# Performance work log

Measured on AMD Instinct MI355X. Metric: run time of the kernel, lower is better.

Reference implementation:

```python
import jax, jax.numpy as jnp
import numpy as np

D_MODEL = 768
N_HEADS = 12
D_HEAD = D_MODEL // N_HEADS
TEMP = float(np.sqrt(D_HEAD))


def setup_inputs() -> dict:
    key = jax.random.key(0)
    ks = jax.random.split(key, 12)
    B, S, D = 8, 2048, D_MODEL
    patches = jax.random.normal(ks[0], (B, S, D), dtype=jnp.float32)
    in_weight = jax.random.uniform(ks[1], (D * 3, D), dtype=jnp.float32)
    in_bias = jax.random.uniform(ks[2], (D * 3,), dtype=jnp.float32)
    out_w = jax.random.normal(ks[3], (D, D), dtype=jnp.float32) * (1.0 / np.sqrt(D))
    out_b = jnp.zeros((D,), dtype=jnp.float32)
    mlp_w1 = jax.random.normal(ks[4], (4 * D, D), dtype=jnp.float32) * (1.0 / np.sqrt(D))
    mlp_b1 = jnp.zeros((4 * D,), dtype=jnp.float32)
    mlp_w2 = jax.random.normal(ks[5], (D, 4 * D), dtype=jnp.float32) * (1.0 / np.sqrt(4 * D))
    mlp_b2 = jnp.zeros((D,), dtype=jnp.float32)
    ln1_g = jnp.ones((D,), dtype=jnp.float32)
    ln1_b = jnp.zeros((D,), dtype=jnp.float32)
    ln2_g = jnp.ones((D,), dtype=jnp.float32)
    ln2_b = jnp.zeros((D,), dtype=jnp.float32)
    return {
        "patches": patches,
        "in_weight": in_weight, "in_bias": in_bias,
        "out_w": out_w, "out_b": out_b,
        "mlp_w1": mlp_w1, "mlp_b1": mlp_b1,
        "mlp_w2": mlp_w2, "mlp_b2": mlp_b2,
        "ln1_g": ln1_g, "ln1_b": ln1_b,
        "ln2_g": ln2_g, "ln2_b": ln2_b,
    }


def layer_norm(x, g, b, eps=1e-5):
    mu = jnp.mean(x, axis=-1, keepdims=True)
    var = jnp.var(x, axis=-1, keepdims=True)
    return (x - mu) * jax.lax.rsqrt(var + eps) * g + b


def mha(x, in_weight, in_bias, out_w, out_b):
    # Replicate quirky per-head reshape: [3D, D] -> [H, d_head, 3, D]
    W = in_weight.reshape(N_HEADS, D_HEAD, 3, D_MODEL)  # h, e, 3, d
    Bv = in_bias.reshape(N_HEADS, D_HEAD, 3)            # h, e, 3
    qw, kw, vw = W[:, :, 0, :], W[:, :, 1, :], W[:, :, 2, :]  # [H, e, D]
    qb, kb, vb = Bv[:, :, 0], Bv[:, :, 1], Bv[:, :, 2]        # [H, e]
    # Q,K,V per head: [B, H, S, e]
    Q = jnp.einsum('bsd,hed->bhse', x, qw) + qb[None, :, None, :]
    K = jnp.einsum('bsd,hed->bhse', x, kw) + kb[None, :, None, :]
    V = jnp.einsum('bsd,hed->bhse', x, vw) + vb[None, :, None, :]
    atn = jnp.einsum('bhse,bhte->bhst', Q, K)
    atn = jax.nn.softmax(atn / TEMP, axis=-1)
    # NOTE: original uses V (not atn @ V) as head output; heads concatenated over feature dim
    B_, H, S, e = V.shape
    heads = jnp.transpose(V, (0, 2, 1, 3)).reshape(B_, S, H * e)
    masks = jnp.sum(atn, axis=1)  # sum over heads: [B, S, S]
    out = heads @ out_w.T + out_b
    return out, masks


def reference(patches, in_weight, in_bias, out_w, out_b,
              mlp_w1, mlp_b1, mlp_w2, mlp_b2,
              ln1_g, ln1_b, ln2_g, ln2_b):
    x = layer_norm(patches, ln1_g, ln1_b)
    sa, _ = mha(x, in_weight, in_bias, out_w, out_b)
    x = sa + x  # dropout = identity (eval)
    x = layer_norm(x, ln2_g, ln2_b)
    h = jax.nn.selu(x @ mlp_w1.T + mlp_b1)
    x = (h @ mlp_w2.T + mlp_b2) + x
    return x
```

## Files before the change

kernel.cpp:

```cpp
#include <hip/hip_runtime.h>


typedef __bf16 bf16;
typedef __bf16 bf16x8 __attribute__((ext_vector_type(8)));
typedef __bf16 bf16x4 __attribute__((ext_vector_type(4)));
typedef float  f32x4  __attribute__((ext_vector_type(4)));

#define N_ROWS  16384

#define AS1(p) ((const __attribute__((address_space(1))) void*)(p))
#define AS3(p) ((__attribute__((address_space(3))) void*)(p))

__global__ __launch_bounds__(256) void cast_kernel(const float* __restrict__ x,
                                                   bf16* __restrict__ y, int n4) {
  int i = blockIdx.x * 256 + threadIdx.x;
  if (i >= n4) return;
  float4 v = ((const float4*)x)[i];
  bf16x4 o = {(bf16)v.x, (bf16)v.y, (bf16)v.z, (bf16)v.w};
  *(bf16x4*)(y + 4 * (size_t)i) = o;
}

__global__ __launch_bounds__(256) void wvt_kernel(const float* __restrict__ in_weight,
                                                  bf16* __restrict__ wvt) {
  int k = blockIdx.x * 256 + threadIdx.x;
  int j = blockIdx.y;
  wvt[(size_t)k * 768 + j] = (bf16)in_weight[((size_t)j * 3 + 2) * 768 + k];
}

__global__ __launch_bounds__(64) void bias_combine_kernel(const float* __restrict__ out_w,
                                                          const float* __restrict__ in_bias,
                                                          const float* __restrict__ out_b,
                                                          float* __restrict__ bc) {
  int n = blockIdx.x, l = threadIdx.x;
  float s = 0.f;
  for (int j = l; j < 768; j += 64) s += out_w[(size_t)n * 768 + j] * in_bias[j * 3 + 2];
#pragma unroll
  for (int off = 32; off > 0; off >>= 1) s += __shfl_xor(s, off, 64);
  if (l == 0) bc[n] = s + out_b[n];
}

__global__ __launch_bounds__(256) void ln_kernel(const float* __restrict__ x,
                                                 const float* __restrict__ g,
                                                 const float* __restrict__ b,
                                                 bf16* __restrict__ y) {
  const int row = blockIdx.x;
  const float* xr = x + (size_t)row * 768;
  float v[3], s1 = 0.f, s2 = 0.f;
#pragma unroll
  for (int i = 0; i < 3; ++i) {
    v[i] = xr[threadIdx.x + i * 256];
    s1 += v[i];
    s2 += v[i] * v[i];
  }
#pragma unroll
  for (int off = 32; off > 0; off >>= 1) {
    s1 += __shfl_xor(s1, off, 64);
    s2 += __shfl_xor(s2, off, 64);
  }
  __shared__ float red[8];
  int w = threadIdx.x >> 6, l = threadIdx.x & 63;
  if (l == 0) { red[w * 2] = s1; red[w * 2 + 1] = s2; }
  __syncthreads();
  s1 = red[0] + red[2] + red[4] + red[6];
  s2 = red[1] + red[3] + red[5] + red[7];
  const float mu = s1 * (1.f / 768.f);
  const float var = s2 * (1.f / 768.f) - mu * mu;
  const float rstd = rsqrtf(var + 1e-5f);
#pragma unroll
  for (int i = 0; i < 3; ++i) {
    int d = threadIdx.x + i * 256;
    y[(size_t)row * 768 + d] = (bf16)((v[i] - mu) * rstd * g[d] + b[d]);
  }
}

template <int EPI>
__global__ __launch_bounds__(256) void gemm_bt(const bf16* __restrict__ A,
                                               const bf16* __restrict__ B,
                                               const float* __restrict__ bias,
                                               const bf16* __restrict__ resid,
                                               void* __restrict__ out,
                                               int M, int N, int K) {
  __shared__ bf16 sA0[128 * 32], sA1[128 * 32];
  __shared__ bf16 sB0[128 * 32], sB1[128 * 32];
  const int tid = threadIdx.x;
  const int w = tid >> 6, l = tid & 63;
  const int wr = w >> 1, wc = w & 1;
  const int q = l >> 4, m16 = l & 15;

  int mtile, ntile;
  {
    const int L = blockIdx.y * gridDim.x + blockIdx.x;
    const int gy = gridDim.y;
    if ((gy & 7) == 0) {
      const int mpx = gy >> 3;
      const int xcd = L & 7;
      const int slot = L >> 3;
      mtile = xcd * mpx + (slot % mpx);
      ntile = slot / mpx;
    } else {
      mtile = blockIdx.y; ntile = blockIdx.x;
    }
  }
  const long tileM = (long)mtile * 128;
  const long tileN = (long)ntile * 128;

  const int ch0 = tid, ch1 = tid + 256;
  const int row0 = ch0 >> 2, row1 = ch1 >> 2;
  const int cl0 = ((ch0 & 3) - (row0 >> 1)) & 3;
  const int cl1 = ((ch1 & 3) - (row1 >> 1)) & 3;
  const bf16* ga0 = A + (tileM + row0) * (long)K + cl0 * 8;
  const bf16* ga1 = A + (tileM + row1) * (long)K + cl1 * 8;
  const bf16* gb0 = B + (tileN + row0) * (long)K + cl0 * 8;
  const bf16* gb1 = B + (tileN + row1) * (long)K + cl1 * 8;
  const int ld0 = ch0 * 8, ld1 = ch1 * 8;

  int offA[4], offB[4];
#pragma unroll
  for (int mi = 0; mi < 4; ++mi) {
    const int r = wr * 64 + mi * 16 + m16;
    offA[mi] = r * 32 + (((q + (r >> 1)) & 3) << 3);
  }
#pragma unroll
  for (int ni = 0; ni < 4; ++ni) {
    const int r = wc * 64 + ni * 16 + m16;
    offB[ni] = r * 32 + (((q + (r >> 1)) & 3) << 3);
  }

  f32x4 acc[4][4] = {};

  __builtin_amdgcn_global_load_lds(AS1(ga0), AS3(&sA0[ld0]), 16, 0, 0);
  __builtin_amdgcn_global_load_lds(AS1(ga1), AS3(&sA0[ld1]), 16, 0, 0);
  __builtin_amdgcn_global_load_lds(AS1(gb0), AS3(&sB0[ld0]), 16, 0, 0);
  __builtin_amdgcn_global_load_lds(AS1(gb1), AS3(&sB0[ld1]), 16, 0, 0);
  __syncthreads();

  const bf16 *cra = sA0, *crb = sB0;
  bf16 *nxa = sA1, *nxb = sB1;

#pragma unroll 2
  for (long k0 = 32; k0 < K; k0 += 32) {
    __builtin_amdgcn_global_load_lds(AS1(ga0 + k0), AS3(&nxa[ld0]), 16, 0, 0);
    __builtin_amdgcn_global_load_lds(AS1(ga1 + k0), AS3(&nxa[ld1]), 16, 0, 0);
    __builtin_amdgcn_global_load_lds(AS1(gb0 + k0), AS3(&nxb[ld0]), 16, 0, 0);
    __builtin_amdgcn_global_load_lds(AS1(gb1 + k0), AS3(&nxb[ld1]), 16, 0, 0);

    bf16x8 af[4], bfr[4];
#pragma unroll
    for (int mi = 0; mi < 4; ++mi) af[mi] = *(const bf16x8*)&cra[offA[mi]];
#pragma unroll
    for (int ni = 0; ni < 4; ++ni) bfr[ni] = *(const bf16x8*)&crb[offB[ni]];
#pragma unroll
    for (int mi = 0; mi < 4; ++mi)
#pragma unroll
      for (int ni = 0; ni < 4; ++ni)
        acc[mi][ni] = __builtin_amdgcn_mfma_f32_16x16x32_bf16(af[mi], bfr[ni],
                                                              acc[mi][ni], 0, 0, 0);

    __syncthreads();

    const bf16* ta = cra; cra = nxa; nxa = (bf16*)ta;
    const bf16* tb = crb; crb = nxb; nxb = (bf16*)tb;
  }

  {
    bf16x8 af[4], bfr[4];
#pragma unroll
    for (int mi = 0; mi < 4; ++mi) af[mi] = *(const bf16x8*)&cra[offA[mi]];
#pragma unroll
    for (int ni = 0; ni < 4; ++ni) bfr[ni] = *(const bf16x8*)&crb[offB[ni]];
#pragma unroll
    for (int mi = 0; mi < 4; ++mi)
#pragma unroll
      for (int ni = 0; ni < 4; ++ni)
        acc[mi][ni] = __builtin_amdgcn_mfma_f32_16x16x32_bf16(af[mi], bfr[ni],
                                                              acc[mi][ni], 0, 0, 0);
  }

  const long colBase = tileN + wc * 64 + m16;
  const long rowBase = tileM + wr * 64 + q * 4;
#pragma unroll
  for (int mi = 0; mi < 4; ++mi) {
#pragma unroll
    for (int r = 0; r < 4; ++r) {
      const long row = rowBase + mi * 16 + r;
#pragma unroll
      for (int ni = 0; ni < 4; ++ni) {
        const long col = colBase + ni * 16;
        float v = acc[mi][ni][r];
        if (EPI == 0) {
          ((bf16*)out)[row * N + col] = (bf16)v;
        } else if (EPI == 1) {
          v += bias[col] + (float)resid[row * N + col];
          ((float*)out)[row * N + col] = v;
        } else {
          v += bias[col];
          v = v > 0.f ? 1.0507009873554805f * v
                      : 1.0507009873554805f * 1.6732632423543772f * (__expf(v) - 1.f);
          ((bf16*)out)[row * N + col] = (bf16)v;
        }
      }
    }
  }
}

extern "C" void kernel_launch(void* const* d_in, const int* in_sizes, int n_in,
                              void* d_out, int out_size, void* d_ws, size_t ws_size,
                              hipStream_t stream) {
  const float* patches   = (const float*)d_in[0];
  const float* in_weight = (const float*)d_in[1];
  const float* in_bias   = (const float*)d_in[2];
  const float* out_w     = (const float*)d_in[3];
  const float* out_b     = (const float*)d_in[4];
  const float* mlp_w1    = (const float*)d_in[5];
  const float* mlp_b1    = (const float*)d_in[6];
  const float* mlp_w2    = (const float*)d_in[7];
  const float* mlp_b2    = (const float*)d_in[8];
  const float* ln1_g     = (const float*)d_in[9];
  const float* ln1_b     = (const float*)d_in[10];
  const float* ln2_g     = (const float*)d_in[11];
  const float* ln2_b     = (const float*)d_in[12];

  char* ws = (char*)d_ws;
  const size_t MB = 1024 * 1024;
  bf16* Wc   = (bf16*)(ws + 0);
  bf16* w1b  = (bf16*)(ws + 2 * MB);
  bf16* w2b  = (bf16*)(ws + 8 * MB);
  bf16* owb  = (bf16*)(ws + 14 * MB);
  bf16* wvt  = (bf16*)(ws + 16 * MB);
  float* bc  = (float*)(ws + 18 * MB);
  bf16* X1   = (bf16*)(ws + 20 * MB);
  bf16* X3   = (bf16*)(ws + 20 * MB);
  bf16* H    = (bf16*)(ws + 48 * MB);
  float* X2  = (float*)d_out;

  cast_kernel<<<(3072 * 768 / 4 + 255) / 256, 256, 0, stream>>>(mlp_w1, w1b, 3072 * 768 / 4);
  cast_kernel<<<(768 * 3072 / 4 + 255) / 256, 256, 0, stream>>>(mlp_w2, w2b, 768 * 3072 / 4);
  cast_kernel<<<(768 * 768 / 4 + 255) / 256, 256, 0, stream>>>(out_w, owb, 768 * 768 / 4);
  wvt_kernel<<<dim3(3, 768), 256, 0, stream>>>(in_weight, wvt);
  bias_combine_kernel<<<768, 64, 0, stream>>>(out_w, in_bias, out_b, bc);
  gemm_bt<0><<<dim3(6, 6), 256, 0, stream>>>(owb, wvt, nullptr, nullptr, Wc, 768, 768, 768);

  ln_kernel<<<N_ROWS, 256, 0, stream>>>(patches, ln1_g, ln1_b, X1);
  gemm_bt<1><<<dim3(6, 128), 256, 0, stream>>>(X1, Wc, bc, X1, X2, N_ROWS, 768, 768);
  ln_kernel<<<N_ROWS, 256, 0, stream>>>(X2, ln2_g, ln2_b, X3);
  gemm_bt<2><<<dim3(24, 128), 256, 0, stream>>>(X3, w1b, mlp_b1, nullptr, H, N_ROWS, 3072, 768);
  gemm_bt<1><<<dim3(6, 128), 256, 0, stream>>>(H, w2b, mlp_b2, X3, d_out, N_ROWS, 768, 3072);
}
```

Measured before the change: 426.8 us.

## Enlarge GEMM block tile to 128x256 with 1x4 warp layout

Each GEMM block now computes a 128x256 output tile instead of 128x128. Each of the four waves owns a 128x64 slab with 8x4 MFMA accumulators, and launch bounds request two blocks per CU. This raises arithmetic intensity per LDS/global load and halves the grid. In exchange it doubles accumulator registers and B-tile LDS, risks spills or lower occupancy, and leaves fewer blocks for the small 768-wide GEMMs.

```diff
diff --git a/kernel.cpp b/kernel.cpp
--- a/kernel.cpp
+++ b/kernel.cpp
@@ -74,17 +74,16 @@
 }
 
 template <int EPI>
-__global__ __launch_bounds__(256) void gemm_bt(const bf16* __restrict__ A,
-                                               const bf16* __restrict__ B,
-                                               const float* __restrict__ bias,
-                                               const bf16* __restrict__ resid,
-                                               void* __restrict__ out,
-                                               int M, int N, int K) {
+__global__ __launch_bounds__(256, 2) void gemm_bt(const bf16* __restrict__ A,
+                                                  const bf16* __restrict__ B,
+                                                  const float* __restrict__ bias,
+                                                  const bf16* __restrict__ resid,
+                                                  void* __restrict__ out,
+                                                  int M, int N, int K) {
   __shared__ bf16 sA0[128 * 32], sA1[128 * 32];
-  __shared__ bf16 sB0[128 * 32], sB1[128 * 32];
+  __shared__ bf16 sB0[256 * 32], sB1[256 * 32];
   const int tid = threadIdx.x;
   const int w = tid >> 6, l = tid & 63;
-  const int wr = w >> 1, wc = w & 1;
   const int q = l >> 4, m16 = l & 15;
 
   int mtile, ntile;
@@ -102,59 +101,71 @@
     }
   }
   const long tileM = (long)mtile * 128;
-  const long tileN = (long)ntile * 128;
-
-  const int ch0 = tid, ch1 = tid + 256;
-  const int row0 = ch0 >> 2, row1 = ch1 >> 2;
-  const int cl0 = ((ch0 & 3) - (row0 >> 1)) & 3;
-  const int cl1 = ((ch1 & 3) - (row1 >> 1)) & 3;
-  const bf16* ga0 = A + (tileM + row0) * (long)K + cl0 * 8;
-  const bf16* ga1 = A + (tileM + row1) * (long)K + cl1 * 8;
-  const bf16* gb0 = B + (tileN + row0) * (long)K + cl0 * 8;
-  const bf16* gb1 = B + (tileN + row1) * (long)K + cl1 * 8;
-  const int ld0 = ch0 * 8, ld1 = ch1 * 8;
-
-  int offA[4], offB[4];
-#pragma unroll
-  for (int mi = 0; mi < 4; ++mi) {
-    const int r = wr * 64 + mi * 16 + m16;
+  const long tileN = (long)ntile * 256;
+
+  const bf16* gA[2]; int ldA[2];
+#pragma unroll
+  for (int i = 0; i < 2; ++i) {
+    const int ch = tid + i * 256;
+    const int row = ch >> 2;
+    const int cl = ((ch & 3) - (row >> 1)) & 3;
+    gA[i] = A + (tileM + row) * (long)K + cl * 8;
+    ldA[i] = ch * 8;
+  }
+  const bf16* gB[4]; int ldB[4];
+#pragma unroll
+  for (int j = 0; j < 4; ++j) {
+    const int ch = tid + j * 256;
+    const int row = ch >> 2;
+    const int cl = ((ch & 3) - (row >> 1)) & 3;
+    gB[j] = B + (tileN + row) * (long)K + cl * 8;
+    ldB[j] = ch * 8;
+  }
+
+  int offA[8], offB[4];
+#pragma unroll
+  for (int mi = 0; mi < 8; ++mi) {
+    const int r = mi * 16 + m16;
     offA[mi] = r * 32 + (((q + (r >> 1)) & 3) << 3);
   }
 #pragma unroll
   for (int ni = 0; ni < 4; ++ni) {
-    const int r = wc * 64 + ni * 16 + m16;
+    const int r = w * 64 + ni * 16 + m16;
     offB[ni] = r * 32 + (((q + (r >> 1)) & 3) << 3);
   }
 
-  f32x4 acc[4][4] = {};
-
-  __builtin_amdgcn_global_load_lds(AS1(ga0), AS3(&sA0[ld0]), 16, 0, 0);
-  __builtin_amdgcn_global_load_lds(AS1(ga1), AS3(&sA0[ld1]), 16, 0, 0);
-  __builtin_amdgcn_global_load_lds(AS1(gb0), AS3(&sB0[ld0]), 16, 0, 0);
-  __builtin_amdgcn_global_load_lds(AS1(gb1), AS3(&sB0[ld1]), 16, 0, 0);
+  f32x4 acc[8][4] = {};
+
+#pragma unroll
+  for (int i = 0; i < 2; ++i)
+    __builtin_amdgcn_global_load_lds(AS1(gA[i]), AS3(&sA0[ldA[i]]), 16, 0, 0);
+#pragma unroll
+  for (int j = 0; j < 4; ++j)
+    __builtin_amdgcn_global_load_lds(AS1(gB[j]), AS3(&sB0[ldB[j]]), 16, 0, 0);
   __syncthreads();
 
   const bf16 *cra = sA0, *crb = sB0;
   bf16 *nxa = sA1, *nxb = sB1;
 
-#pragma unroll 2
   for (long k0 = 32; k0 < K; k0 += 32) {
-    __builtin_amdgcn_global_load_lds(AS1(ga0 + k0), AS3(&nxa[ld0]), 16, 0, 0);
-    __builtin_amdgcn_global_load_lds(AS1(ga1 + k0), AS3(&nxa[ld1]), 16, 0, 0);
-    __builtin_amdgcn_global_load_lds(AS1(gb0 + k0), AS3(&nxb[ld0]), 16, 0, 0);
-    __builtin_amdgcn_global_load_lds(AS1(gb1 + k0), AS3(&nxb[ld1]), 16, 0, 0);
-
-    bf16x8 af[4], bfr[4];
-#pragma unroll
-    for (int mi = 0; mi < 4; ++mi) af[mi] = *(const bf16x8*)&cra[offA[mi]];
+#pragma unroll
+    for (int i = 0; i < 2; ++i)
+      __builtin_amdgcn_global_load_lds(AS1(gA[i] + k0), AS3(&nxa[ldA[i]]), 16, 0, 0);
+#pragma unroll
+    for (int j = 0; j < 4; ++j)
+      __builtin_amdgcn_global_load_lds(AS1(gB[j] + k0), AS3(&nxb[ldB[j]]), 16, 0, 0);
+
+    bf16x8 bfr[4];
 #pragma unroll
     for (int ni = 0; ni < 4; ++ni) bfr[ni] = *(const bf16x8*)&crb[offB[ni]];
 #pragma unroll
-    for (int mi = 0; mi < 4; ++mi)
+    for (int mi = 0; mi < 8; ++mi) {
+      const bf16x8 af = *(const bf16x8*)&cra[offA[mi]];
 #pragma unroll
       for (int ni = 0; ni < 4; ++ni)
-        acc[mi][ni] = __builtin_amdgcn_mfma_f32_16x16x32_bf16(af[mi], bfr[ni],
+        acc[mi][ni] = __builtin_amdgcn_mfma_f32_16x16x32_bf16(af, bfr[ni],
                                                               acc[mi][ni], 0, 0, 0);
+    }
 
     __syncthreads();
 
@@ -163,23 +174,23 @@
   }
 
   {
-    bf16x8 af[4], bfr[4];
-#pragma unroll
-    for (int mi = 0; mi < 4; ++mi) af[mi] = *(const bf16x8*)&cra[offA[mi]];
+    bf16x8 bfr[4];
 #pragma unroll
     for (int ni = 0; ni < 4; ++ni) bfr[ni] = *(const bf16x8*)&crb[offB[ni]];
 #pragma unroll
-    for (int mi = 0; mi < 4; ++mi)
+    for (int mi = 0; mi < 8; ++mi) {
+      const bf16x8 af = *(const bf16x8*)&cra[offA[mi]];
 #pragma unroll
       for (int ni = 0; ni < 4; ++ni)
-        acc[mi][ni] = __builtin_amdgcn_mfma_f32_16x16x32_bf16(af[mi], bfr[ni],
+        acc[mi][ni] = __builtin_amdgcn_mfma_f32_16x16x32_bf16(af, bfr[ni],
                                                               acc[mi][ni], 0, 0, 0);
-  }
-
-  const long colBase = tileN + wc * 64 + m16;
-  const long rowBase = tileM + wr * 64 + q * 4;
-#pragma unroll
-  for (int mi = 0; mi < 4; ++mi) {
+    }
+  }
+
+  const long colBase = tileN + (long)w * 64 + m16;
+  const long rowBase = tileM + q * 4;
+#pragma unroll
+  for (int mi = 0; mi < 8; ++mi) {
 #pragma unroll
     for (int r = 0; r < 4; ++r) {
       const long row = rowBase + mi * 16 + r;
@@ -238,11 +249,11 @@
   cast_kernel<<<(768 * 768 / 4 + 255) / 256, 256, 0, stream>>>(out_w, owb, 768 * 768 / 4);
   wvt_kernel<<<dim3(3, 768), 256, 0, stream>>>(in_weight, wvt);
   bias_combine_kernel<<<768, 64, 0, stream>>>(out_w, in_bias, out_b, bc);
-  gemm_bt<0><<<dim3(6, 6), 256, 0, stream>>>(owb, wvt, nullptr, nullptr, Wc, 768, 768, 768);
+  gemm_bt<0><<<dim3(3, 6), 256, 0, stream>>>(owb, wvt, nullptr, nullptr, Wc, 768, 768, 768);
 
   ln_kernel<<<N_ROWS, 256, 0, stream>>>(patches, ln1_g, ln1_b, X1);
-  gemm_bt<1><<<dim3(6, 128), 256, 0, stream>>>(X1, Wc, bc, X1, X2, N_ROWS, 768, 768);
+  gemm_bt<1><<<dim3(3, 128), 256, 0, stream>>>(X1, Wc, bc, X1, X2, N_ROWS, 768, 768);
   ln_kernel<<<N_ROWS, 256, 0, stream>>>(X2, ln2_g, ln2_b, X3);
-  gemm_bt<2><<<dim3(24, 128), 256, 0, stream>>>(X3, w1b, mlp_b1, nullptr, H, N_ROWS, 3072, 768);
-  gemm_bt<1><<<dim3(6, 128), 256, 0, stream>>>(H, w2b, mlp_b2, X3, d_out, N_ROWS, 768, 3072);
-}
+  gemm_bt<2><<<dim3(12, 128), 256, 0, stream>>>(X3, w1b, mlp_b1, nullptr, H, N_ROWS, 3072, 768);
+  gemm_bt<1><<<dim3(3, 128), 256, 0, stream>>>(H, w2b, mlp_b2, X3, d_out, N_ROWS, 768, 3072);
+}
```

Measured after the change: 409.2 us. 4.1% less time.
